# Performance work log

Hardware: AMD Instinct MI355X
Metric: run time of the kernel (lower is better)

Reference implementation:

```python
import jax, jax.numpy as jnp
import numpy as np

B, N, K = 4096, 87, 87


def setup_inputs() -> dict:
    key = jax.random.key(0)
    ks = jax.random.split(key, 6)
    x = jax.random.normal(ks[0], (B, N, N), dtype=jnp.float32)
    evals = jax.random.uniform(ks[1], (B, K), dtype=jnp.float32)
    evecs = jax.random.normal(ks[2], (B, N, K), dtype=jnp.float32)
    # learned per-node diffusion times (torch inits to 0, clamped to 1e-8;
    # use small positive values to exercise the exp decay)
    diffusion_time = jax.random.uniform(ks[3], (N,), dtype=jnp.float32) * 0.1
    # MiniMLP: single Linear(2*N -> N)
    lim = 1.0 / np.sqrt(2 * N)
    W = jax.random.uniform(ks[4], (N, 2 * N), minval=-lim, maxval=lim, dtype=jnp.float32)
    b = jax.random.uniform(ks[5], (N,), minval=-lim, maxval=lim, dtype=jnp.float32)
    return {"x": x, "evals": evals, "evecs": evecs,
            "diffusion_time": diffusion_time, "W": W, "b": b}


def reference(x, evals, evecs, diffusion_time, W, b):
    # clamp diffusion times (torch does this in-place on .data)
    t = jnp.maximum(diffusion_time, 1e-8)                     # (N,)
    # expa[b,i,m] = exp(-t_i * eval[b,m])
    expa = jnp.exp(-t[None, :, None] * evals[:, None, :])     # (B,N,K)
    # kernel[b,i,j] = sum_m evec[b,i,m] * expa[b,i,m] * evec[b,j,m]
    # (equivalent to the diag_embed + triple matmul + diagonal in the torch code)
    kernel = jnp.einsum('bim,bjm->bij', evecs * expa, evecs)  # (B,N,N)
    x_diffuse = jnp.concatenate([x, kernel], axis=2)          # (B,N,2N)
    return x_diffuse @ W.T + b                                # (B,N,N)
```

## Files before the change

kernel.cpp:

```cpp
#include <hip/hip_runtime.h>
#include <hip/hip_bf16.h>
#include <math.h>

#define NN    87
#define NN2   (NN * NN)
#define EPW   92
#define EPN   (96 * EPW + 4)
#define XPW   92
#define XPN   (96 * XPW + 16)
#define WPH   104
#define WPANEL (96 * WPH)
#define NT    256

#define WS_W     0
#define WS_EPAD  (2 * WPANEL * 2)
#define EPAD_N   8360
#define WS_NEED  (WS_EPAD + EPAD_N * 4)

typedef __attribute__((ext_vector_type(8))) short bf16x8;
typedef __attribute__((ext_vector_type(4))) short bf16x4;
typedef __attribute__((ext_vector_type(4))) float f32x4;
typedef float f32x4u __attribute__((ext_vector_type(4), aligned(4)));

__device__ __forceinline__ short f2bf(float f) {
    __hip_bfloat16 h = __float2bfloat16(f);
    return *(short*)&h;
}

__device__ __forceinline__ void gl16(const float* g, float* l) {
    __builtin_amdgcn_global_load_lds(
        (const __attribute__((address_space(1))) void*)g,
        (__attribute__((address_space(3))) void*)l, 16, 0, 0);
}

__global__ void prep(const float* __restrict__ W, const float* __restrict__ evecs,
                     int B, char* __restrict__ ws)
{
    int idx = (int)blockIdx.x * NT + (int)threadIdx.x;
    short* wp = (short*)(ws + WS_W);
    float* ep = (float*)(ws + WS_EPAD);
    if (idx < 2 * WPANEL) {
        int p = idx / WPANEL, rem = idx - p * WPANEL;
        int r = rem / WPH, c = rem - r * WPH;
        short v = 0;
        if (r < NN && c < NN) v = f2bf(W[r * (2 * NN) + p * NN + c]);
        wp[idx] = v;
    }
    int i2 = idx - 2 * WPANEL;
    if (i2 >= 0 && i2 < EPAD_N)
        ep[i2] = (i2 < NN2) ? evecs[(size_t)(B - 1) * NN2 + i2] : 0.f;
}

template <bool WS>
__device__ __forceinline__ bf16x8 wload(const short* __restrict__ wp,
                                        const float* __restrict__ gW,
                                        int panel, int jrow, int jcl, int k0, bool tailKs)
{
    if constexpr (WS) {
        return *(const bf16x8*)&wp[panel * WPANEL + jrow * WPH + k0];
    } else {
        float v[8];
        if (!tailKs) {
            f32x4u a  = *(const f32x4u*)(gW + jcl * (2 * NN) + panel * NN + k0);
            f32x4u b4 = *(const f32x4u*)(gW + jcl * (2 * NN) + panel * NN + k0 + 4);
            v[0] = a.x; v[1] = a.y; v[2] = a.z; v[3] = a.w;
            v[4] = b4.x; v[5] = b4.y; v[6] = b4.z; v[7] = b4.w;
        } else {
            #pragma unroll
            for (int q = 0; q < 8; ++q) {
                int k = k0 + q;
                v[q] = (k < NN) ? gW[jcl * (2 * NN) + panel * NN + k] : 0.f;
            }
        }
        bf16x8 o;
        #pragma unroll
        for (int q = 0; q < 8; ++q) o[q] = f2bf(v[q]);
        return o;
    }
}

template <bool WS>
__global__ __launch_bounds__(NT, 3)
void fused(const float* __restrict__ gx, const float* __restrict__ gevals,
           const float* __restrict__ gevecs, const float* __restrict__ dtime,
           const float* __restrict__ gW, const float* __restrict__ bias,
           const char* __restrict__ ws, int B, float* __restrict__ out)
{
    __shared__ __align__(16) float sE[EPN];
    __shared__ __align__(16) short sX[XPN];
    __shared__ float sLam[96];
    short* const sD = (short*)sE;
    float* const sF = (float*)sE;

    const int b    = (int)blockIdx.x;
    const int tid  = (int)threadIdx.x;
    const int lane = tid & 63;
    const int wave = tid >> 6;
    const int l15  = lane & 15;
    const int lk   = lane >> 4;
    const int i0   = (wave >> 1) * 48;
    const int j0   = (wave & 1) * 48;

    const float* __restrict__ Eb = gevecs + (size_t)b * NN2;
    const float* __restrict__ xb = gx     + (size_t)b * NN2;
    const short* wp = nullptr;
    if constexpr (WS) {
        wp = (const short*)(ws + WS_W);
        if (b == B - 1) Eb = (const float*)(ws + WS_EPAD);
    }

    if (tid < 96) sLam[tid] = (tid < NN) ? gevals[(size_t)b * NN + tid] : 3e38f;

    int ir[3], jr[3];
    float tr_[3];
    #pragma unroll
    for (int r = 0; r < 3; ++r) {
        ir[r] = i0 + 16 * r + l15;
        jr[r] = j0 + 16 * r + l15;
        tr_[r] = fmaxf(dtime[ir[r] < NN ? ir[r] : NN - 1], 1e-8f);
    }

    if (tid < 4)  sE[96 * EPW + tid] = 0.f;
    if (tid < 16) sX[96 * XPW + tid] = 0;
    for (int u = tid; u < 96 * 5; u += NT) {
        int r = u / 5, c = NN + u % 5;
        sX[r * XPW + c] = 0;
    }
    for (int u = tid; u < 9 * NN; u += NT) {
        int r = NN + u / NN, c = u % NN;
        sX[r * XPW + c] = 0;
    }

    if constexpr (WS) {
        for (int vc = wave; vc < 35; vc += 4) {
            int p  = vc * 256 + lane * 4;
            int row = p / EPW;
            int col = p - row * EPW;
            const float* g = Eb + row * NN + col;
            if (vc < 34) gl16(g, &sE[vc * 256]);
            else if (lane < 32) gl16(g, &sE[vc * 256]);
        }
    } else {
        for (int u = tid; u < NN * 22; u += NT) {
            int r = u / 22, sg = u - r * 22, c = sg * 4;
            const float* pE = Eb + r * NN + c;
            if (sg < 21) *(f32x4*)&sE[r * EPW + c] = *(const f32x4u*)pE;
            else { f32x4 t; t.x = pE[0]; t.y = pE[1]; t.z = pE[2]; t.w = 0.f;
                   *(f32x4*)&sE[r * EPW + c] = t; }
        }
        for (int u = tid; u < 96 * 4; u += NT) {
            int r = u >> 2, c = 88 + (u & 3);
            sE[r * EPW + c] = 0.f;
        }
        for (int u = tid; u < 9 * 88; u += NT) {
            int r = NN + u / 88, c = u % 88;
            sE[r * EPW + c] = 0.f;
        }
    }

    float xq[8][4];
    float x7568 = 0.f;
    #pragma unroll
    for (int k = 0; k < 8; ++k) {
        int u = tid + k * NT;
        int uc = (u < 1892) ? u : 1891;
        f32x4u t = *(const f32x4u*)(xb + 4 * uc);
        xq[k][0] = t.x; xq[k][1] = t.y; xq[k][2] = t.z; xq[k][3] = t.w;
    }
    if (tid == 0) x7568 = xb[7568];

    if constexpr (WS) {
        asm volatile("s_waitcnt vmcnt(8) lgkmcnt(0)" ::: "memory");
        __builtin_amdgcn_s_barrier();
        __builtin_amdgcn_sched_barrier(0);
    } else {
        __syncthreads();
    }

    f32x4 acc1[3][3];
    #pragma unroll
    for (int c = 0; c < 3; ++c)
        #pragma unroll
        for (int r = 0; r < 3; ++r) acc1[c][r] = (f32x4){0.f, 0.f, 0.f, 0.f};

    #pragma unroll
    for (int ks = 0; ks < 3; ++ks) {
        const int k0 = ks * 32 + lk * 8;
        f32x4 la  = *(const f32x4*)&sLam[k0];
        f32x4 lb4 = *(const f32x4*)&sLam[k0 + 4];
        float l8_[8] = {la.x, la.y, la.z, la.w, lb4.x, lb4.y, lb4.z, lb4.w};

        bf16x8 ef[3], af[3];
        #pragma unroll
        for (int c = 0; c < 3; ++c) {
            f32x4 lo = *(const f32x4*)&sE[jr[c] * EPW + k0];
            f32x4 hi = *(const f32x4*)&sE[jr[c] * EPW + k0 + 4];
            #pragma unroll
            for (int q = 0; q < 4; ++q) { ef[c][q] = f2bf(lo[q]); ef[c][q + 4] = f2bf(hi[q]); }
        }
        #pragma unroll
        for (int r = 0; r < 3; ++r) {
            f32x4 lo = *(const f32x4*)&sE[ir[r] * EPW + k0];
            f32x4 hi = *(const f32x4*)&sE[ir[r] * EPW + k0 + 4];
            #pragma unroll
            for (int q = 0; q < 4; ++q) {
                af[r][q]     = f2bf(lo[q] * __expf(-tr_[r] * l8_[q]));
                af[r][q + 4] = f2bf(hi[q] * __expf(-tr_[r] * l8_[q + 4]));
            }
        }
        #pragma unroll
        for (int c = 0; c < 3; ++c)
            #pragma unroll
            for (int r = 0; r < 3; ++r)
                acc1[c][r] = __builtin_amdgcn_mfma_f32_16x16x32_bf16(ef[c], af[r], acc1[c][r], 0, 0, 0);
    }
    __syncthreads();

    #pragma unroll
    for (int c = 0; c < 3; ++c) {
        const int jb = j0 + 16 * c + lk * 4;
        if (jb < 92) {
            #pragma unroll
            for (int r = 0; r < 3; ++r) {
                const int i = i0 + 16 * r + l15;
                bf16x4 v = {f2bf(acc1[c][r][0]), f2bf(acc1[c][r][1]),
                            f2bf(acc1[c][r][2]), f2bf(acc1[c][r][3])};
                *(bf16x4*)&sD[i * XPW + jb] = v;
            }
        }
    }
    if (tid < 4) sD[96 * XPW + tid] = 0;
    __builtin_amdgcn_sched_barrier(0);

    #pragma unroll
    for (int k = 0; k < 8; ++k) {
        int u = tid + k * NT;
        if (u < 1892) {
            int f = 4 * u;
            #pragma unroll
            for (int e = 0; e < 4; ++e) {
                int fe = f + e;
                if (fe < NN2) {
                    int r = fe / NN, c = fe - r * NN;
                    sX[r * XPW + c] = f2bf(xq[k][e]);
                }
            }
        }
    }
    if (tid == 0) sX[86 * XPW + 86] = f2bf(x7568);

    bf16x8 wfx[3][3], wfd[3][3];
    #pragma unroll
    for (int ks = 0; ks < 3; ++ks)
        #pragma unroll
        for (int wr = 0; wr < 3; ++wr) {
            int jc = jr[wr] < NN ? jr[wr] : NN - 1;
            wfx[ks][wr] = wload<WS>(wp, gW, 0, jr[wr], jc, ks * 32 + lk * 8, ks == 2);
            wfd[ks][wr] = wload<WS>(wp, gW, 1, jr[wr], jc, ks * 32 + lk * 8, ks == 2);
        }
    __syncthreads();

    f32x4 acc2[3][3];
    #pragma unroll
    for (int wr = 0; wr < 3; ++wr)
        #pragma unroll
        for (int xc = 0; xc < 3; ++xc) acc2[wr][xc] = (f32x4){0.f, 0.f, 0.f, 0.f};

    #pragma unroll
    for (int ks = 0; ks < 3; ++ks) {
        const int k0 = ks * 32 + lk * 8;
        bf16x8 xf[3];
        #pragma unroll
        for (int xc = 0; xc < 3; ++xc) {
            bf16x4 lo = *(const bf16x4*)&sX[ir[xc] * XPW + k0];
            bf16x4 hi = *(const bf16x4*)&sX[ir[xc] * XPW + k0 + 4];
            #pragma unroll
            for (int q = 0; q < 4; ++q) { xf[xc][q] = lo[q]; xf[xc][q + 4] = hi[q]; }
        }
        #pragma unroll
        for (int wr = 0; wr < 3; ++wr)
            #pragma unroll
            for (int xc = 0; xc < 3; ++xc)
                acc2[wr][xc] = __builtin_amdgcn_mfma_f32_16x16x32_bf16(wfx[ks][wr], xf[xc], acc2[wr][xc], 0, 0, 0);
    }
    #pragma unroll
    for (int ks = 0; ks < 3; ++ks) {
        const int k0 = ks * 32 + lk * 8;
        bf16x8 df[3];
        #pragma unroll
        for (int xc = 0; xc < 3; ++xc) {
            bf16x4 lo = *(const bf16x4*)&sD[ir[xc] * XPW + k0];
            bf16x4 hi = *(const bf16x4*)&sD[ir[xc] * XPW + k0 + 4];
            #pragma unroll
            for (int q = 0; q < 4; ++q) { df[xc][q] = lo[q]; df[xc][q + 4] = hi[q]; }
        }
        #pragma unroll
        for (int wr = 0; wr < 3; ++wr)
            #pragma unroll
            for (int xc = 0; xc < 3; ++xc)
                acc2[wr][xc] = __builtin_amdgcn_mfma_f32_16x16x32_bf16(wfd[ks][wr], df[xc], acc2[wr][xc], 0, 0, 0);
    }
    __syncthreads();

    #pragma unroll
    for (int wr = 0; wr < 3; ++wr) {
        const int jb = j0 + 16 * wr + lk * 4;
        float bj[4];
        if (jb + 3 < NN) {
            f32x4u t = *(const f32x4u*)(bias + jb);
            bj[0] = t.x; bj[1] = t.y; bj[2] = t.z; bj[3] = t.w;
        } else {
            #pragma unroll
            for (int q = 0; q < 4; ++q) bj[q] = (jb + q < NN) ? bias[jb + q] : 0.f;
        }
        #pragma unroll
        for (int xc = 0; xc < 3; ++xc) {
            const int i = i0 + 16 * xc + l15;
            #pragma unroll
            for (int q = 0; q < 4; ++q) {
                const int j = jb + q;
                if (j < NN) sF[i * NN + j] = acc2[wr][xc][q] + bj[q];
            }
        }
    }
    __syncthreads();

    {
        float* __restrict__ gb = out + (size_t)b * NN2;
        const int s = (4 - ((b * NN2) & 3)) & 3;
        if (tid < s) gb[tid] = sF[tid];
        const int C = (NN2 - s) >> 2;
        for (int m = tid; m < C; m += NT) {
            const int n = s + 4 * m;
            f32x4 v;
            v.x = sF[n]; v.y = sF[n + 1]; v.z = sF[n + 2]; v.w = sF[n + 3];
            *(f32x4*)(gb + n) = v;
        }
        const int tl = s + 4 * C;
        if (tid < NN2 - tl) gb[tl + tid] = sF[tl + tid];
    }
}

extern "C" void kernel_launch(void* const* d_in, const int* in_sizes, int n_in,
                              void* d_out, int out_size, void* d_ws, size_t ws_size,
                              hipStream_t stream)
{
    const float* x     = (const float*)d_in[0];
    const float* evals = (const float*)d_in[1];
    const float* evecs = (const float*)d_in[2];
    const float* dtime = (const float*)d_in[3];
    const float* W     = (const float*)d_in[4];
    const float* bias  = (const float*)d_in[5];
    float* out = (float*)d_out;

    const int B = in_sizes[1] / NN;

    if (ws_size >= (size_t)WS_NEED) {
        const int prep_elems = 2 * WPANEL + EPAD_N;
        prep<<<(prep_elems + NT - 1) / NT, NT, 0, stream>>>(W, evecs, B, (char*)d_ws);
        fused<true><<<dim3(B), dim3(NT), 0, stream>>>(x, evals, evecs, dtime, W, bias,
                                                      (const char*)d_ws, B, out);
    } else {
        fused<false><<<dim3(B), dim3(NT), 0, stream>>>(x, evals, evecs, dtime, W, bias,
                                                       nullptr, B, out);
    }
}
```

Measured before the change: 96.00 us.

## Alias bf16 X/D tiles into the evec LDS buffer and defer W loads

Removes the separate sX shared buffer by placing both bf16 tiles (kernel result sD and input sX) inside the existing float sE region, using row stride EPW. This cuts LDS per block. Launch bounds go from 3 to 4 blocks per CU. The second-panel W fragments are now loaded inside the D-panel k-loop instead of up front, which lowers register pressure so the higher occupancy fits. The padding zero-fill for sX moves after the sE reads finish. In exchange, W loads in the second GEMM stage are no longer hidden behind earlier work, and the aliasing depends on sE being dead before it is overwritten.

Result: faster. 93.03 us (-3.1%).

```diff
diff --git a/kernel.cpp b/kernel.cpp
--- a/kernel.cpp
+++ b/kernel.cpp
@@ -6,8 +6,6 @@
 #define NN2   (NN * NN)
 #define EPW   92
 #define EPN   (96 * EPW + 4)
-#define XPW   92
-#define XPN   (96 * XPW + 16)
 #define WPH   104
 #define WPANEL (96 * WPH)
 #define NT    256
@@ -80,16 +78,16 @@
 }
 
 template <bool WS>
-__global__ __launch_bounds__(NT, 3)
+__global__ __launch_bounds__(NT, 4)
 void fused(const float* __restrict__ gx, const float* __restrict__ gevals,
            const float* __restrict__ gevecs, const float* __restrict__ dtime,
            const float* __restrict__ gW, const float* __restrict__ bias,
            const char* __restrict__ ws, int B, float* __restrict__ out)
 {
     __shared__ __align__(16) float sE[EPN];
-    __shared__ __align__(16) short sX[XPN];
     __shared__ float sLam[96];
     short* const sD = (short*)sE;
+    short* const sX = sD + 96 * EPW;
     float* const sF = (float*)sE;
 
     const int b    = (int)blockIdx.x;
@@ -120,20 +118,11 @@
         tr_[r] = fmaxf(dtime[ir[r] < NN ? ir[r] : NN - 1], 1e-8f);
     }
 
-    if (tid < 4)  sE[96 * EPW + tid] = 0.f;
-    if (tid < 16) sX[96 * XPW + tid] = 0;
-    for (int u = tid; u < 96 * 5; u += NT) {
-        int r = u / 5, c = NN + u % 5;
-        sX[r * XPW + c] = 0;
-    }
-    for (int u = tid; u < 9 * NN; u += NT) {
-        int r = NN + u / NN, c = u % NN;
-        sX[r * XPW + c] = 0;
-    }
+    if (tid < 4) sE[96 * EPW + tid] = 0.f;
 
     if constexpr (WS) {
         for (int vc = wave; vc < 35; vc += 4) {
-            int p  = vc * 256 + lane * 4;
+            int p   = vc * 256 + lane * 4;
             int row = p / EPW;
             int col = p - row * EPW;
             const float* g = Eb + row * NN + col;
@@ -219,17 +208,16 @@
     #pragma unroll
     for (int c = 0; c < 3; ++c) {
         const int jb = j0 + 16 * c + lk * 4;
-        if (jb < 92) {
+        if (jb < EPW) {
             #pragma unroll
             for (int r = 0; r < 3; ++r) {
                 const int i = i0 + 16 * r + l15;
                 bf16x4 v = {f2bf(acc1[c][r][0]), f2bf(acc1[c][r][1]),
                             f2bf(acc1[c][r][2]), f2bf(acc1[c][r][3])};
-                *(bf16x4*)&sD[i * XPW + jb] = v;
-            }
-        }
-    }
-    if (tid < 4) sD[96 * XPW + tid] = 0;
+                *(bf16x4*)&sD[i * EPW + jb] = v;
+            }
+        }
+    }
     __builtin_amdgcn_sched_barrier(0);
 
     #pragma unroll
@@ -242,21 +230,28 @@
                 int fe = f + e;
                 if (fe < NN2) {
                     int r = fe / NN, c = fe - r * NN;
-                    sX[r * XPW + c] = f2bf(xq[k][e]);
+                    sX[r * EPW + c] = f2bf(xq[k][e]);
                 }
             }
         }
     }
-    if (tid == 0) sX[86 * XPW + 86] = f2bf(x7568);
-
-    bf16x8 wfx[3][3], wfd[3][3];
+    if (tid == 0) sX[86 * EPW + 86] = f2bf(x7568);
+    for (int u = tid; u < 96 * 5; u += NT) {
+        int r = u / 5, c = NN + u % 5;
+        sX[r * EPW + c] = 0;
+    }
+    for (int u = tid; u < 9 * NN; u += NT) {
+        int r = NN + u / NN, c = u % NN;
+        sX[r * EPW + c] = 0;
+    }
+
+    bf16x8 wfx[3][3];
     #pragma unroll
     for (int ks = 0; ks < 3; ++ks)
         #pragma unroll
         for (int wr = 0; wr < 3; ++wr) {
             int jc = jr[wr] < NN ? jr[wr] : NN - 1;
             wfx[ks][wr] = wload<WS>(wp, gW, 0, jr[wr], jc, ks * 32 + lk * 8, ks == 2);
-            wfd[ks][wr] = wload<WS>(wp, gW, 1, jr[wr], jc, ks * 32 + lk * 8, ks == 2);
         }
     __syncthreads();
 
@@ -272,8 +267,8 @@
         bf16x8 xf[3];
         #pragma unroll
         for (int xc = 0; xc < 3; ++xc) {
-            bf16x4 lo = *(const bf16x4*)&sX[ir[xc] * XPW + k0];
-            bf16x4 hi = *(const bf16x4*)&sX[ir[xc] * XPW + k0 + 4];
+            bf16x4 lo = *(const bf16x4*)&sX[ir[xc] * EPW + k0];
+            bf16x4 hi = *(const bf16x4*)&sX[ir[xc] * EPW + k0 + 4];
             #pragma unroll
             for (int q = 0; q < 4; ++q) { xf[xc][q] = lo[q]; xf[xc][q + 4] = hi[q]; }
         }
@@ -286,11 +281,16 @@
     #pragma unroll
     for (int ks = 0; ks < 3; ++ks) {
         const int k0 = ks * 32 + lk * 8;
-        bf16x8 df[3];
+        bf16x8 wfd[3], df[3];
+        #pragma unroll
+        for (int wr = 0; wr < 3; ++wr) {
+            int jc = jr[wr] < NN ? jr[wr] : NN - 1;
+            wfd[wr] = wload<WS>(wp, gW, 1, jr[wr], jc, k0, ks == 2);
+        }
         #pragma unroll
         for (int xc = 0; xc < 3; ++xc) {
-            bf16x4 lo = *(const bf16x4*)&sD[ir[xc] * XPW + k0];
-            bf16x4 hi = *(const bf16x4*)&sD[ir[xc] * XPW + k0 + 4];
+            bf16x4 lo = *(const bf16x4*)&sD[ir[xc] * EPW + k0];
+            bf16x4 hi = *(const bf16x4*)&sD[ir[xc] * EPW + k0 + 4];
             #pragma unroll
             for (int q = 0; q < 4; ++q) { df[xc][q] = lo[q]; df[xc][q + 4] = hi[q]; }
         }
@@ -298,7 +298,7 @@
         for (int wr = 0; wr < 3; ++wr)
             #pragma unroll
             for (int xc = 0; xc < 3; ++xc)
-                acc2[wr][xc] = __builtin_amdgcn_mfma_f32_16x16x32_bf16(wfd[ks][wr], df[xc], acc2[wr][xc], 0, 0, 0);
+                acc2[wr][xc] = __builtin_amdgcn_mfma_f32_16x16x32_bf16(wfd[wr], df[xc], acc2[wr][xc], 0, 0, 0);
     }
     __syncthreads();
 
```
